# Kernel optimization log

Hardware: AMD Instinct MI355X
Metric: run time of the kernel (lower is better)

Reference implementation:

```python
import jax, jax.numpy as jnp
import numpy as np

B, IN, OUT = 512, 4096, 11008


def setup_inputs() -> dict:
    key = jax.random.key(0)
    k_x, k_stored, k_sign, k_scale, k_bias = jax.random.split(key, 5)
    x = jax.random.normal(k_x, (B, IN), dtype=jnp.float32)
    # QINS encoding: stored uint8 magnitude in [1, 255], sign in {-1, +1}
    stored = jax.random.randint(k_stored, (OUT, IN), 1, 256, dtype=jnp.int32)
    sign = 2 * jax.random.randint(k_sign, (OUT, IN), 0, 2, dtype=jnp.int32) - 1
    # log-range from from_linear's fallback calibration: weights in [e^-10, e^0]
    log_min = jnp.asarray(-10.0, dtype=jnp.float32)
    log_max = jnp.asarray(0.0, dtype=jnp.float32)
    # per-channel calibration scale, clamped to [0.5, 2.0] in from_linear
    scale = jax.random.uniform(k_scale, (OUT,), dtype=jnp.float32, minval=0.5, maxval=2.0)
    bias = jax.random.normal(k_bias, (OUT,), dtype=jnp.float32) * 0.01
    return {"x": x, "stored": stored, "sign": sign, "log_min": log_min,
            "log_max": log_max, "scale": scale, "bias": bias}


def reference(x, stored, sign, log_min, log_max, scale, bias):
    # Reconstruct fp32 weight from log-scale uint8 encoding (QINS)
    normalized = (255.0 - stored.astype(jnp.float32)) / 254.0      # [OUT, IN]
    log_w = log_min + normalized * (log_max - log_min)
    weight = sign.astype(jnp.float32) * jnp.exp(log_w)             # [OUT, IN]
    # y = (x @ W^T + b) * scale   (per-output-channel scale)
    out = jnp.einsum('bi,oi->bo', x, weight) + bias
    return out * scale
```

## Files before the change

kernel.cpp:

```cpp
#include <hip/hip_runtime.h>
#include <hip/hip_bf16.h>

#define B_DIM   512
#define IN_DIM  4096
#define OUT_DIM 11008

typedef __bf16 bf16x4 __attribute__((ext_vector_type(4)));
typedef __bf16 bf16x8 __attribute__((ext_vector_type(8)));
typedef float  floatx4 __attribute__((ext_vector_type(4)));

__global__ __launch_bounds__(256) void conv_x_kernel(
    const float* __restrict__ x, __bf16* __restrict__ xb) {
  int idx = blockIdx.x * blockDim.x + threadIdx.x;
  float4 v = ((const float4*)x)[idx];
  bf16x4 o;
  o[0] = (__bf16)v.x; o[1] = (__bf16)v.y; o[2] = (__bf16)v.z; o[3] = (__bf16)v.w;
  ((bf16x4*)xb)[idx] = o;
}

__device__ __forceinline__ void gl_lds16(const __bf16* g, __bf16* l) {
  __builtin_amdgcn_global_load_lds(
      (const __attribute__((address_space(1))) void*)g,
      (__attribute__((address_space(3))) void*)l, 16, 0, 0);
}

__global__ __launch_bounds__(512, 2) void fused_gemm_kernel(
    const __bf16* __restrict__ A,
    const int* __restrict__ stored,
    const int* __restrict__ sign,
    const float* __restrict__ logmin, const float* __restrict__ logmax,
    const float* __restrict__ scale, const float* __restrict__ bias,
    float* __restrict__ out) {
  constexpr int K = IN_DIM, N = OUT_DIM;
  constexpr int BK = 32;

  __shared__ __align__(16) __bf16 sA[512 * BK];
  __shared__ __align__(16) __bf16 sB[64 * BK];

  const int tid  = threadIdx.x;
  const int lane = tid & 63;
  const int wave = tid >> 6;
  const int m16  = lane & 15;
  const int q    = lane >> 4;

  const int bn0 = blockIdx.x * 64;

  const float lmin  = logmin[0];
  const float slope = (logmax[0] - lmin) * (1.0f / 254.0f);

  const int ar = tid >> 2;
  const int ac = (tid & 3) * 8;
  const __bf16* gA = A + (size_t)ar * K + ac;
  __bf16* lA = sA + tid * 8;

  const int br = tid >> 3;
  const int bc = (tid & 7) * 4;
  const int* gS = stored + (size_t)(bn0 + br) * K + bc;
  const int* gG = sign   + (size_t)(bn0 + br) * K + bc;
  __bf16* lB = sB + tid * 4;

  floatx4 acc[4][4] = {};

  for (int kt = 0; kt < K; kt += BK) {
    int4 s = *(const int4*)(gS + kt);
    int4 g = *(const int4*)(gG + kt);

    __syncthreads();

    gl_lds16(gA + kt,             lA);
    gl_lds16(gA + kt + 128 * K,   lA + 4096);
    gl_lds16(gA + kt + 256 * K,   lA + 8192);
    gl_lds16(gA + kt + 384 * K,   lA + 12288);

    bf16x4 wv;
    wv[0] = (__bf16)(__expf(lmin + (float)(255 - s.x) * slope) * (float)g.x);
    wv[1] = (__bf16)(__expf(lmin + (float)(255 - s.y) * slope) * (float)g.y);
    wv[2] = (__bf16)(__expf(lmin + (float)(255 - s.z) * slope) * (float)g.z);
    wv[3] = (__bf16)(__expf(lmin + (float)(255 - s.w) * slope) * (float)g.w);
    *(bf16x4*)lB = wv;

    __syncthreads();

    bf16x8 afr[4], bfr[4];
#pragma unroll
    for (int i = 0; i < 4; ++i)
      afr[i] = *(const bf16x8*)&sA[(wave * 64 + i * 16 + m16) * BK + q * 8];
#pragma unroll
    for (int i = 0; i < 4; ++i)
      bfr[i] = *(const bf16x8*)&sB[(i * 16 + m16) * BK + q * 8];

#pragma unroll
    for (int mi = 0; mi < 4; ++mi)
#pragma unroll
      for (int ni = 0; ni < 4; ++ni)
        acc[mi][ni] = __builtin_amdgcn_mfma_f32_16x16x32_bf16(
            afr[mi], bfr[ni], acc[mi][ni], 0, 0, 0);
  }

#pragma unroll
  for (int ni = 0; ni < 4; ++ni) {
    const int col = bn0 + ni * 16 + m16;
    const float sc = scale[col];
    const float bb = bias[col] * sc;
#pragma unroll
    for (int mi = 0; mi < 4; ++mi) {
#pragma unroll
      for (int r = 0; r < 4; ++r) {
        const int row = wave * 64 + mi * 16 + q * 4 + r;
        out[(size_t)row * N + col] = acc[mi][ni][r] * sc + bb;
      }
    }
  }
}

extern "C" void kernel_launch(void* const* d_in, const int* in_sizes, int n_in,
                              void* d_out, int out_size, void* d_ws, size_t ws_size,
                              hipStream_t stream) {
  const float* x      = (const float*)d_in[0];
  const int*   stored = (const int*)d_in[1];
  const int*   sign   = (const int*)d_in[2];
  const float* logmin = (const float*)d_in[3];
  const float* logmax = (const float*)d_in[4];
  const float* scale  = (const float*)d_in[5];
  const float* bias   = (const float*)d_in[6];
  float* out = (float*)d_out;

  __bf16* wsX = (__bf16*)d_ws;

  conv_x_kernel<<<(B_DIM * (IN_DIM / 4)) / 256, 256, 0, stream>>>(x, wsX);
  fused_gemm_kernel<<<OUT_DIM / 64, 512, 0, stream>>>(
      wsX, stored, sign, logmin, logmax, scale, bias, out);
}
```

Baseline: 476.7 us.

## Load A fragments directly to registers and double-buffer decoded weights with prefetch

Drops the shared-memory staging of the activation tile. Each wave now loads its A fragments straight from global memory into registers, one k-step ahead. Decoded weights go into a double-buffered LDS tile, so only one barrier per iteration is needed. The stored and sign loads are prefetched two steps ahead using nontemporal loads. This removes the LDS round trip for A and one sync, at the cost of more registers and uncoalesced per-lane global reads of A.

```diff
diff --git a/kernel.cpp b/kernel.cpp
--- a/kernel.cpp
+++ b/kernel.cpp
@@ -5,9 +5,10 @@
 #define IN_DIM  4096
 #define OUT_DIM 11008
 
-typedef __bf16 bf16x4 __attribute__((ext_vector_type(4)));
-typedef __bf16 bf16x8 __attribute__((ext_vector_type(8)));
+typedef __bf16 bf16x4  __attribute__((ext_vector_type(4)));
+typedef __bf16 bf16x8  __attribute__((ext_vector_type(8)));
 typedef float  floatx4 __attribute__((ext_vector_type(4)));
+typedef int    intx4   __attribute__((ext_vector_type(4)));
 
 __global__ __launch_bounds__(256) void conv_x_kernel(
     const float* __restrict__ x, __bf16* __restrict__ xb) {
@@ -16,12 +17,6 @@
   bf16x4 o;
   o[0] = (__bf16)v.x; o[1] = (__bf16)v.y; o[2] = (__bf16)v.z; o[3] = (__bf16)v.w;
   ((bf16x4*)xb)[idx] = o;
-}
-
-__device__ __forceinline__ void gl_lds16(const __bf16* g, __bf16* l) {
-  __builtin_amdgcn_global_load_lds(
-      (const __attribute__((address_space(1))) void*)g,
-      (__attribute__((address_space(3))) void*)l, 16, 0, 0);
 }
 
 __global__ __launch_bounds__(512, 2) void fused_gemm_kernel(
@@ -34,8 +29,7 @@
   constexpr int K = IN_DIM, N = OUT_DIM;
   constexpr int BK = 32;
 
-  __shared__ __align__(16) __bf16 sA[512 * BK];
-  __shared__ __align__(16) __bf16 sB[64 * BK];
+  __shared__ __align__(16) __bf16 sB[2][64 * BK];
 
   const int tid  = threadIdx.x;
   const int lane = tid & 63;
@@ -48,53 +42,78 @@
   const float lmin  = logmin[0];
   const float slope = (logmax[0] - lmin) * (1.0f / 254.0f);
 
-  const int ar = tid >> 2;
-  const int ac = (tid & 3) * 8;
-  const __bf16* gA = A + (size_t)ar * K + ac;
-  __bf16* lA = sA + tid * 8;
-
   const int br = tid >> 3;
   const int bc = (tid & 7) * 4;
   const int* gS = stored + (size_t)(bn0 + br) * K + bc;
   const int* gG = sign   + (size_t)(bn0 + br) * K + bc;
-  __bf16* lB = sB + tid * 4;
+
+  const __bf16* gA = A + (size_t)(wave * 64 + m16) * K + q * 8;
 
   floatx4 acc[4][4] = {};
 
-  for (int kt = 0; kt < K; kt += BK) {
-    int4 s = *(const int4*)(gS + kt);
-    int4 g = *(const int4*)(gG + kt);
+#define DECODE_STORE(sv, gv, dst)                                              \
+  {                                                                            \
+    bf16x4 wv;                                                                 \
+    wv[0] = (__bf16)(__expf(fmaf((float)(255 - (sv).x), slope, lmin)) *        \
+                     (float)(gv).x);                                           \
+    wv[1] = (__bf16)(__expf(fmaf((float)(255 - (sv).y), slope, lmin)) *        \
+                     (float)(gv).y);                                           \
+    wv[2] = (__bf16)(__expf(fmaf((float)(255 - (sv).z), slope, lmin)) *        \
+                     (float)(gv).z);                                           \
+    wv[3] = (__bf16)(__expf(fmaf((float)(255 - (sv).w), slope, lmin)) *        \
+                     (float)(gv).w);                                           \
+    *(bf16x4*)(dst) = wv;                                                      \
+  }
 
+  intx4 sv = __builtin_nontemporal_load((const intx4*)(gS));
+  intx4 gv = __builtin_nontemporal_load((const intx4*)(gG));
+  bf16x8 afrA[4];
+#pragma unroll
+  for (int i = 0; i < 4; ++i)
+    afrA[i] = *(const bf16x8*)(gA + (size_t)(i * 16) * K);
+  DECODE_STORE(sv, gv, &sB[0][tid * 4]);
+  intx4 s0 = __builtin_nontemporal_load((const intx4*)(gS + BK));
+  intx4 g0 = __builtin_nontemporal_load((const intx4*)(gG + BK));
+  intx4 s1 = __builtin_nontemporal_load((const intx4*)(gS + 2 * BK));
+  intx4 g1 = __builtin_nontemporal_load((const intx4*)(gG + 2 * BK));
+
+  int p = 0;
+  for (int kt = 0; kt < K; kt += BK, p ^= 1) {
     __syncthreads();
 
-    gl_lds16(gA + kt,             lA);
-    gl_lds16(gA + kt + 128 * K,   lA + 4096);
-    gl_lds16(gA + kt + 256 * K,   lA + 8192);
-    gl_lds16(gA + kt + 384 * K,   lA + 12288);
+    const bool more = (kt + BK) < K;
 
-    bf16x4 wv;
-    wv[0] = (__bf16)(__expf(lmin + (float)(255 - s.x) * slope) * (float)g.x);
-    wv[1] = (__bf16)(__expf(lmin + (float)(255 - s.y) * slope) * (float)g.y);
-    wv[2] = (__bf16)(__expf(lmin + (float)(255 - s.z) * slope) * (float)g.z);
-    wv[3] = (__bf16)(__expf(lmin + (float)(255 - s.w) * slope) * (float)g.w);
-    *(bf16x4*)lB = wv;
+    bf16x8 afrB[4];
+    if (more) {
+#pragma unroll
+      for (int i = 0; i < 4; ++i)
+        afrB[i] = *(const bf16x8*)(gA + (size_t)(i * 16) * K + kt + BK);
+    }
 
-    __syncthreads();
-
-    bf16x8 afr[4], bfr[4];
+    bf16x8 bfr[4];
 #pragma unroll
     for (int i = 0; i < 4; ++i)
-      afr[i] = *(const bf16x8*)&sA[(wave * 64 + i * 16 + m16) * BK + q * 8];
-#pragma unroll
-    for (int i = 0; i < 4; ++i)
-      bfr[i] = *(const bf16x8*)&sB[(i * 16 + m16) * BK + q * 8];
+      bfr[i] = *(const bf16x8*)&sB[p][(i * 16 + m16) * BK + q * 8];
+
+    if (more) {
+      DECODE_STORE(s0, g0, &sB[p ^ 1][tid * 4]);
+      s0 = s1; g0 = g1;
+      const int kt3 = (kt + 3 * BK) < K ? (kt + 3 * BK) : 0;
+      s1 = __builtin_nontemporal_load((const intx4*)(gS + kt3));
+      g1 = __builtin_nontemporal_load((const intx4*)(gG + kt3));
+    }
 
 #pragma unroll
     for (int mi = 0; mi < 4; ++mi)
 #pragma unroll
       for (int ni = 0; ni < 4; ++ni)
         acc[mi][ni] = __builtin_amdgcn_mfma_f32_16x16x32_bf16(
-            afr[mi], bfr[ni], acc[mi][ni], 0, 0, 0);
+            afrA[mi], bfr[ni], acc[mi][ni], 0, 0, 0);
+
+    if (more) {
+#pragma unroll
+      for (int i = 0; i < 4; ++i) afrA[i] = afrB[i];
+    }
   }
 
 #pragma unroll
@@ -111,6 +130,7 @@
       }
     }
   }
+#undef DECODE_STORE
 }
 
 extern "C" void kernel_launch(void* const* d_in, const int* in_sizes, int n_in,
```

New measurement: 530.7 us. +11.3%, slower.
